# Performance work log

Measured on AMD Instinct MI355X. Metric: run time of the kernel, lower is better.

## Reference

```python
import jax, jax.numpy as jnp
import numpy as np

B, N, T = 64, 325, 12
HID = 64        # hidden_size of each expert
MEM_HID = 32    # mem_hid
MEM_SZ = 20     # memory_size
IN_DIM = 3      # input_dim
E = 3           # number of experts (len of hid_query/key/value lists)
COS_EPS = 1e-8  # torch.nn.CosineSimilarity default eps


def _xavier(key, shape):
    fan_in, fan_out = shape[-2], shape[-1]
    limit = float(np.sqrt(6.0 / (fan_in + fan_out)))
    return jax.random.uniform(key, shape, jnp.float32, -limit, limit)


def setup_inputs() -> dict:
    key = jax.random.key(0)
    ks = jax.random.split(key, 10)
    inp = {
        "input": jax.random.normal(ks[0], (B, N, T, IN_DIM), jnp.float32),
        "hidden0": jax.random.normal(ks[1], (B, N, T, HID), jnp.float32),
        "hidden1": jax.random.normal(ks[2], (B, N, T, HID), jnp.float32),
        "hidden2": jax.random.normal(ks[3], (B, N, T, HID), jnp.float32),
        # learned parameters (xavier_uniform init as in the module)
        "memory": _xavier(ks[4], (MEM_SZ, MEM_HID)),
        "input_query": _xavier(ks[5], (IN_DIM, MEM_HID)),
        # stacked per-expert projection matrices: [E, HID, MEM_HID]
        "hid_query": _xavier(ks[6], (E, HID, MEM_HID)),
        "key_w": _xavier(ks[7], (E, HID, MEM_HID)),
        "value_w": _xavier(ks[8], (E, HID, MEM_HID)),
    }
    return inp


def _cosine_sim(a, b):
    # torch CosineSimilarity(dim=-1): dot / max(||a||*||b||, eps)
    dot = jnp.sum(a * b, axis=-1)
    na = jnp.linalg.norm(a, axis=-1)
    nb = jnp.linalg.norm(b, axis=-1)
    return dot / jnp.maximum(na * nb, COS_EPS)


def reference(input, hidden0, hidden1, hidden2, memory, input_query, hid_query, key_w, value_w):
    # --- query_mem: memory-augmented representation of the raw input ---
    q = jnp.einsum('bnti,im->bntm', input, input_query)          # [B,N,T,MEM_HID]
    mem_score = jax.nn.softmax(jnp.einsum('bntm,sm->bnts', q, memory), axis=-1)
    memories = jnp.einsum('bnts,sm->bntm', mem_score, memory)    # [B,N,T,MEM_HID]

    # --- per-expert temporal self-attention in mem_hid space (vectorized over experts) ---
    h = jnp.stack([hidden0, hidden1, hidden2], axis=0)           # [E,B,N,T,HID]
    Q = jnp.einsum('ebntc,ecm->ebntm', h, hid_query)
    K = jnp.einsum('ebntc,ecm->ebntm', h, key_w)
    V = jnp.einsum('ebntc,ecm->ebntm', h, value_w)
    energy = jnp.einsum('ebntm,ebnsm->ebnts', Q, K)              # [E,B,N,T,T]
    attn = jax.nn.softmax(energy, axis=-1)
    hidden_att = jnp.einsum('ebnts,ebnsm->ebntm', attn, V)       # [E,B,N,T,MEM_HID]

    # --- cosine similarity routing scores, stacked over experts ---
    scores = _cosine_sim(memories[None], hidden_att)             # [E,B,N,T]
    return jnp.moveaxis(scores, 0, -1)                           # [B,N,T,E]
```

## Files before the change

kernel.cpp:

```cpp
#include <hip/hip_runtime.h>
#include <math.h>

typedef __attribute__((ext_vector_type(8))) short short8;
typedef __attribute__((ext_vector_type(4))) short short4v;
typedef __attribute__((ext_vector_type(4))) float f32x4;

namespace {

constexpr int kT = 12, kMS = 20, kE = 3;
constexpr int kSites = 64 * 325;
constexpr int kWaves = 8;
constexpr int kThreads = kWaves * 64;
constexpr int kNB = 340;
constexpr int kStride = kNB * kWaves;
constexpr int kIters = (kSites + kStride - 1) / kStride;

__device__ __forceinline__ void split1(float x, unsigned& hi, unsigned& lo) {
  unsigned u = __float_as_uint(x);
  hi = u >> 16;
  float r = x - __uint_as_float(u & 0xFFFF0000u);
  lo = __float_as_uint(r) >> 16;
}
__device__ __forceinline__ float btrunc(float x) {
  return __uint_as_float(__float_as_uint(x) & 0xFFFF0000u);
}
__device__ __forceinline__ unsigned pk_hi(float a, float b) {
  return __builtin_amdgcn_perm(__float_as_uint(b), __float_as_uint(a), 0x07060302u);
}
__device__ __forceinline__ unsigned pk_rnd(float a, float b) {
  return __builtin_amdgcn_perm(__float_as_uint(b) + 0x8000u,
                               __float_as_uint(a) + 0x8000u, 0x07060302u);
}

union S8 { short8 s; unsigned u[4]; };
union S4 { short4v s; unsigned u[2]; };

#define MFMA32(a, b, c) __builtin_amdgcn_mfma_f32_16x16x32_bf16((a), (b), (c), 0, 0, 0)
#define MFMA16(a, b, c) __builtin_amdgcn_mfma_f32_16x16x16bf16_1k((a), (b), (c), 0, 0, 0)

__global__ __launch_bounds__(kThreads, 4) void testam_mfma(
    const float* __restrict__ input, const float* __restrict__ h0,
    const float* __restrict__ h1, const float* __restrict__ h2,
    const float* __restrict__ memw, const float* __restrict__ iq,
    const float* __restrict__ hq, const float* __restrict__ kwt,
    const float* __restrict__ vw, float* __restrict__ out) {

  __shared__ __align__(16) unsigned short wlds[2][12][512];
  __shared__ __align__(16) float Glds[32][4];

  const int tid = threadIdx.x;
  const int e = blockIdx.x / kNB;
  const int b = blockIdx.x % kNB;
  const int l = tid & 63, wv = tid >> 6;
  const int g = l >> 4, c = l & 15;

  for (int idx = tid; idx < 768; idx += kThreads) {
    int ll = idx & 63, fi = idx >> 6;
    int mat = fi >> 2, x = (fi >> 1) & 1, y = fi & 1;
    int gg = ll >> 4, cc = ll & 15;
    const float* wp = ((mat == 0) ? hq : (mat == 1) ? kwt : vw) + e * 2048
                      + (y * 32 + gg * 8) * 32 + x * 16 + cc;
    short8 sh, sl;
    #pragma unroll
    for (int j = 0; j < 8; ++j) {
      unsigned h, lo; split1(wp[j * 32], h, lo);
      sh[j] = (short)h; sl[j] = (short)lo;
    }
    *(short8*)&wlds[0][fi][ll * 8] = sh;
    *(short8*)&wlds[1][fi][ll * 8] = sl;
  }
  for (int idx = tid; idx < 128; idx += kThreads) {
    int s = idx >> 2, d = idx & 3;
    float acc = 0.f;
    if (d < 3 && s < kMS) {
      for (int m = 0; m < 32; ++m) acc += iq[d * 32 + m] * memw[s * 32 + m];
    }
    Glds[s][d] = acc;
  }

  S4 mwh[2][2], mwl[2][2];
  #pragma unroll
  for (int p = 0; p < 2; ++p)
    #pragma unroll
    for (int sch = 0; sch < 2; ++sch) {
      float v[4];
      #pragma unroll
      for (int j = 0; j < 4; ++j) {
        int s = 16 * sch + 4 * g + j;
        v[j] = (s < kMS) ? memw[s * 32 + 16 * p + c] : 0.f;
      }
      mwh[p][sch].u[0] = pk_hi(v[0], v[1]);
      mwh[p][sch].u[1] = pk_hi(v[2], v[3]);
      mwl[p][sch].u[0] = pk_hi(v[0] - btrunc(v[0]), v[1] - btrunc(v[1]));
      mwl[p][sch].u[1] = pk_hi(v[2] - btrunc(v[2]), v[3] - btrunc(v[3]));
    }
  __syncthreads();

  const float* hbase = (e == 0) ? h0 : (e == 1) ? h1 : h2;
  const f32x4 fz = {0.f, 0.f, 0.f, 0.f};

  const int crow = (c < kT) ? c : 0;

  auto load_site = [&](int s, float* hr, float* pr) {
    const int sc_ = (s < kSites) ? s : (kSites - 1);
    const float* p = hbase + (size_t)sc_ * 768 + crow * 64 + g * 8;
    *(f32x4*)&hr[0]  = *(const f32x4*)&p[0];
    *(f32x4*)&hr[4]  = *(const f32x4*)&p[4];
    *(f32x4*)&hr[8]  = *(const f32x4*)&p[32];
    *(f32x4*)&hr[12] = *(const f32x4*)&p[36];
    const float* ip = input + (size_t)sc_ * 36 + crow * 3;
    pr[0] = ip[0]; pr[1] = ip[1]; pr[2] = ip[2];
  };

  auto body = [&](int site, const float* hv, const float* pv) {
    S8 ah[2], al[2];
    #pragma unroll
    for (int k0i = 0; k0i < 2; ++k0i)
      #pragma unroll
      for (int jj = 0; jj < 4; ++jj) {
        float a = hv[k0i * 8 + 2 * jj], bb = hv[k0i * 8 + 2 * jj + 1];
        ah[k0i].u[jj] = pk_hi(a, bb);
        al[k0i].u[jj] = pk_hi(a - btrunc(a), bb - btrunc(bb));
      }

    f32x4 cq[2] = {fz, fz}, ck[2] = {fz, fz}, cv[2] = {fz, fz};
    __builtin_amdgcn_s_setprio(1);
    #pragma unroll
    for (int p = 0; p < 2; ++p)
      #pragma unroll
      for (int k0i = 0; k0i < 2; ++k0i) {
        {
          const int fi = 0 + p * 2 + k0i;
          short8 wh = *(const short8*)&wlds[0][fi][l * 8];
          short8 wlo = *(const short8*)&wlds[1][fi][l * 8];
          cq[p] = MFMA32(wh, ah[k0i].s, cq[p]);
          cq[p] = MFMA32(wh, al[k0i].s, cq[p]);
          cq[p] = MFMA32(wlo, ah[k0i].s, cq[p]);
        }
        {
          const int fi = 4 + p * 2 + k0i;
          short8 wh = *(const short8*)&wlds[0][fi][l * 8];
          short8 wlo = *(const short8*)&wlds[1][fi][l * 8];
          ck[p] = MFMA32(wh, ah[k0i].s, ck[p]);
          ck[p] = MFMA32(wh, al[k0i].s, ck[p]);
          ck[p] = MFMA32(wlo, ah[k0i].s, ck[p]);
        }
        {
          const int fi = 8 + p * 2 + k0i;
          short8 wh = *(const short8*)&wlds[0][fi][l * 8];
          short8 wlo = *(const short8*)&wlds[1][fi][l * 8];
          cv[p] = MFMA32(ah[k0i].s, wh, cv[p]);
          cv[p] = MFMA32(ah[k0i].s, wlo, cv[p]);
          cv[p] = MFMA32(al[k0i].s, wh, cv[p]);
        }
      }
    __builtin_amdgcn_s_setprio(0);

    S4 cqh[2], cql[2], ckh[2], ckl[2], va[2];
    #pragma unroll
    for (int p = 0; p < 2; ++p) {
      cqh[p].u[0] = pk_hi(cq[p][0], cq[p][1]);
      cqh[p].u[1] = pk_hi(cq[p][2], cq[p][3]);
      cql[p].u[0] = pk_hi(cq[p][0] - btrunc(cq[p][0]), cq[p][1] - btrunc(cq[p][1]));
      cql[p].u[1] = pk_hi(cq[p][2] - btrunc(cq[p][2]), cq[p][3] - btrunc(cq[p][3]));
      ckh[p].u[0] = pk_hi(ck[p][0], ck[p][1]);
      ckh[p].u[1] = pk_hi(ck[p][2], ck[p][3]);
      ckl[p].u[0] = pk_hi(ck[p][0] - btrunc(ck[p][0]), ck[p][1] - btrunc(ck[p][1]));
      ckl[p].u[1] = pk_hi(ck[p][2] - btrunc(ck[p][2]), ck[p][3] - btrunc(ck[p][3]));
      va[p].u[0] = pk_rnd(cv[p][0], cv[p][1]);
      va[p].u[1] = pk_rnd(cv[p][2], cv[p][3]);
    }

    f32x4 eng = fz;
    #pragma unroll
    for (int p = 0; p < 2; ++p) {
      eng = MFMA16(ckh[p].s, cqh[p].s, eng);
      eng = MFMA16(ckh[p].s, cql[p].s, eng);
      eng = MFMA16(ckl[p].s, cqh[p].s, eng);
    }

    float w[4];
    {
      float mloc = -1e30f;
      if (g < 3) {
        mloc = eng[0];
        #pragma unroll
        for (int r = 1; r < 4; ++r) mloc = fmaxf(mloc, eng[r]);
      }
      float mx = mloc;
      mx = fmaxf(mx, __shfl_xor(mx, 16));
      mx = fmaxf(mx, __shfl_xor(mx, 32));
      float sloc = 0.f;
      #pragma unroll
      for (int r = 0; r < 4; ++r) {
        w[r] = (g < 3) ? __expf(eng[r] - mx) : 0.f;
        sloc += w[r];
      }
      float sm = sloc;
      sm += __shfl_xor(sm, 16);
      sm += __shfl_xor(sm, 32);
      float inv = 1.f / sm;
      #pragma unroll
      for (int r = 0; r < 4; ++r) w[r] *= inv;
    }

    S4 wh_, wl_;
    wh_.u[0] = pk_hi(w[0], w[1]);
    wh_.u[1] = pk_hi(w[2], w[3]);
    wl_.u[0] = pk_hi(w[0] - btrunc(w[0]), w[1] - btrunc(w[1]));
    wl_.u[1] = pk_hi(w[2] - btrunc(w[2]), w[3] - btrunc(w[3]));
    f32x4 hat[2];
    #pragma unroll
    for (int p = 0; p < 2; ++p) {
      hat[p] = MFMA16(va[p].s, wh_.s, fz);
      hat[p] = MFMA16(va[p].s, wl_.s, hat[p]);
    }

    float sc0[4], sc1[4];
    #pragma unroll
    for (int r = 0; r < 4; ++r) {
      const f32x4 Gv0 = *(const f32x4*)&Glds[4 * g + r][0];
      sc0[r] = pv[0] * Gv0[0] + pv[1] * Gv0[1] + pv[2] * Gv0[2];
      const f32x4 Gv1 = *(const f32x4*)&Glds[16 + 4 * g + r][0];
      sc1[r] = pv[0] * Gv1[0] + pv[1] * Gv1[1] + pv[2] * Gv1[2];
    }
    float w0[4], w1[4];
    {
      float mloc = sc0[0];
      #pragma unroll
      for (int r = 1; r < 4; ++r) mloc = fmaxf(mloc, sc0[r]);
      if (g == 0) {
        #pragma unroll
        for (int r = 0; r < 4; ++r) mloc = fmaxf(mloc, sc1[r]);
      }
      float mx = mloc;
      mx = fmaxf(mx, __shfl_xor(mx, 16));
      mx = fmaxf(mx, __shfl_xor(mx, 32));
      float sloc = 0.f;
      #pragma unroll
      for (int r = 0; r < 4; ++r) {
        w0[r] = __expf(sc0[r] - mx); sloc += w0[r];
        w1[r] = (g == 0) ? __expf(sc1[r] - mx) : 0.f; sloc += w1[r];
      }
      float sm = sloc;
      sm += __shfl_xor(sm, 16);
      sm += __shfl_xor(sm, 32);
      float inv = 1.f / sm;
      #pragma unroll
      for (int r = 0; r < 4; ++r) { w0[r] *= inv; w1[r] *= inv; }
    }

    S4 w0h, w0l, w1h, w1l;
    w0h.u[0] = pk_hi(w0[0], w0[1]);  w0h.u[1] = pk_hi(w0[2], w0[3]);
    w0l.u[0] = pk_hi(w0[0] - btrunc(w0[0]), w0[1] - btrunc(w0[1]));
    w0l.u[1] = pk_hi(w0[2] - btrunc(w0[2]), w0[3] - btrunc(w0[3]));
    w1h.u[0] = pk_hi(w1[0], w1[1]);  w1h.u[1] = pk_hi(w1[2], w1[3]);
    w1l.u[0] = pk_hi(w1[0] - btrunc(w1[0]), w1[1] - btrunc(w1[1]));
    w1l.u[1] = pk_hi(w1[2] - btrunc(w1[2]), w1[3] - btrunc(w1[3]));
    f32x4 cmem[2];
    #pragma unroll
    for (int p = 0; p < 2; ++p) {
      cmem[p] = MFMA16(mwh[p][0].s, w0h.s, fz);
      cmem[p] = MFMA16(mwh[p][0].s, w0l.s, cmem[p]);
      cmem[p] = MFMA16(mwl[p][0].s, w0h.s, cmem[p]);
      cmem[p] = MFMA16(mwh[p][1].s, w1h.s, cmem[p]);
      cmem[p] = MFMA16(mwh[p][1].s, w1l.s, cmem[p]);
      cmem[p] = MFMA16(mwl[p][1].s, w1h.s, cmem[p]);
    }

    float dot = 0.f, na = 0.f, nb = 0.f;
    #pragma unroll
    for (int p = 0; p < 2; ++p)
      #pragma unroll
      for (int r = 0; r < 4; ++r) {
        float a = cmem[p][r], h = hat[p][r];
        dot += a * h; na += a * a; nb += h * h;
      }
    dot += __shfl_xor(dot, 16); dot += __shfl_xor(dot, 32);
    na  += __shfl_xor(na, 16);  na  += __shfl_xor(na, 32);
    nb  += __shfl_xor(nb, 16);  nb  += __shfl_xor(nb, 32);
    if (g == 0 && c < kT) {
      float cvv = dot / fmaxf(sqrtf(na) * sqrtf(nb), 1e-8f);
      out[(size_t)site * (kT * kE) + c * kE + e] = cvv;
    }
  };

  float hA[16], hB[16], pA[3], pB[3];
  int site = b * kWaves + wv;
  load_site(site, hA, pA);
  for (int it = 0; it < kIters; it += 2) {
    load_site(site + kStride, hB, pB);
    if (site < kSites) body(site, hA, pA);
    load_site(site + 2 * kStride, hA, pA);
    const int s2 = site + kStride;
    if (s2 < kSites) body(s2, hB, pB);
    site += 2 * kStride;
  }
}

}

extern "C" void kernel_launch(void* const* d_in, const int* in_sizes, int n_in,
                              void* d_out, int out_size, void* d_ws, size_t ws_size,
                              hipStream_t stream) {
  const float* input = (const float*)d_in[0];
  const float* h0    = (const float*)d_in[1];
  const float* h1    = (const float*)d_in[2];
  const float* h2    = (const float*)d_in[3];
  const float* memw  = (const float*)d_in[4];
  const float* iq    = (const float*)d_in[5];
  const float* hq    = (const float*)d_in[6];
  const float* kw    = (const float*)d_in[7];
  const float* vw    = (const float*)d_in[8];
  float* out = (float*)d_out;

  testam_mfma<<<kE * kNB, kThreads, 0, stream>>>(
      input, h0, h1, h2, memw, iq, hq, kw, vw, out);
}
```

Baseline: 74.32 us.

## Process all three experts per site in one block and share the memory-branch result

```diff
diff --git a/kernel.cpp b/kernel.cpp
--- a/kernel.cpp
+++ b/kernel.cpp
@@ -11,7 +11,7 @@
 constexpr int kSites = 64 * 325;
 constexpr int kWaves = 8;
 constexpr int kThreads = kWaves * 64;
-constexpr int kNB = 340;
+constexpr int kNB = 512;
 constexpr int kStride = kNB * kWaves;
 constexpr int kIters = (kSites + kStride - 1) / kStride;
 
@@ -45,20 +45,20 @@
     const float* __restrict__ hq, const float* __restrict__ kwt,
     const float* __restrict__ vw, float* __restrict__ out) {
 
-  __shared__ __align__(16) unsigned short wlds[2][12][512];
+  __shared__ __align__(16) unsigned short wlds[kE][2][12][512];
   __shared__ __align__(16) float Glds[32][4];
 
   const int tid = threadIdx.x;
-  const int e = blockIdx.x / kNB;
-  const int b = blockIdx.x % kNB;
+  const int b = blockIdx.x;
   const int l = tid & 63, wv = tid >> 6;
   const int g = l >> 4, c = l & 15;
 
-  for (int idx = tid; idx < 768; idx += kThreads) {
-    int ll = idx & 63, fi = idx >> 6;
+  for (int idx = tid; idx < kE * 768; idx += kThreads) {
+    int e2 = idx / 768, rem = idx - e2 * 768;
+    int ll = rem & 63, fi = rem >> 6;
     int mat = fi >> 2, x = (fi >> 1) & 1, y = fi & 1;
     int gg = ll >> 4, cc = ll & 15;
-    const float* wp = ((mat == 0) ? hq : (mat == 1) ? kwt : vw) + e * 2048
+    const float* wp = ((mat == 0) ? hq : (mat == 1) ? kwt : vw) + e2 * 2048
                       + (y * 32 + gg * 8) * 32 + x * 16 + cc;
     short8 sh, sl;
     #pragma unroll
@@ -66,8 +66,8 @@
       unsigned h, lo; split1(wp[j * 32], h, lo);
       sh[j] = (short)h; sl[j] = (short)lo;
     }
-    *(short8*)&wlds[0][fi][ll * 8] = sh;
-    *(short8*)&wlds[1][fi][ll * 8] = sl;
+    *(short8*)&wlds[e2][0][fi][ll * 8] = sh;
+    *(short8*)&wlds[e2][1][fi][ll * 8] = sl;
   }
   for (int idx = tid; idx < 128; idx += kThreads) {
     int s = idx >> 2, d = idx & 3;
@@ -96,23 +96,77 @@
     }
   __syncthreads();
 
-  const float* hbase = (e == 0) ? h0 : (e == 1) ? h1 : h2;
   const f32x4 fz = {0.f, 0.f, 0.f, 0.f};
 
   const int crow = (c < kT) ? c : 0;
 
-  auto load_site = [&](int s, float* hr, float* pr) {
+  auto load_h = [&](const float* hb, int s, float* hr) {
     const int sc_ = (s < kSites) ? s : (kSites - 1);
-    const float* p = hbase + (size_t)sc_ * 768 + crow * 64 + g * 8;
+    const float* p = hb + (size_t)sc_ * 768 + crow * 64 + g * 8;
     *(f32x4*)&hr[0]  = *(const f32x4*)&p[0];
     *(f32x4*)&hr[4]  = *(const f32x4*)&p[4];
     *(f32x4*)&hr[8]  = *(const f32x4*)&p[32];
     *(f32x4*)&hr[12] = *(const f32x4*)&p[36];
+  };
+  auto load_p = [&](int s, float* pr) {
+    const int sc_ = (s < kSites) ? s : (kSites - 1);
     const float* ip = input + (size_t)sc_ * 36 + crow * 3;
     pr[0] = ip[0]; pr[1] = ip[1]; pr[2] = ip[2];
   };
 
-  auto body = [&](int site, const float* hv, const float* pv) {
+  auto memfn = [&](const float* pv, f32x4* cmem) {
+    float sc0[4], sc1[4];
+    #pragma unroll
+    for (int r = 0; r < 4; ++r) {
+      const f32x4 Gv0 = *(const f32x4*)&Glds[4 * g + r][0];
+      sc0[r] = pv[0] * Gv0[0] + pv[1] * Gv0[1] + pv[2] * Gv0[2];
+      const f32x4 Gv1 = *(const f32x4*)&Glds[16 + 4 * g + r][0];
+      sc1[r] = pv[0] * Gv1[0] + pv[1] * Gv1[1] + pv[2] * Gv1[2];
+    }
+    float w0[4], w1[4];
+    {
+      float mloc = sc0[0];
+      #pragma unroll
+      for (int r = 1; r < 4; ++r) mloc = fmaxf(mloc, sc0[r]);
+      if (g == 0) {
+        #pragma unroll
+        for (int r = 0; r < 4; ++r) mloc = fmaxf(mloc, sc1[r]);
+      }
+      float mx = mloc;
+      mx = fmaxf(mx, __shfl_xor(mx, 16));
+      mx = fmaxf(mx, __shfl_xor(mx, 32));
+      float sloc = 0.f;
+      #pragma unroll
+      for (int r = 0; r < 4; ++r) {
+        w0[r] = __expf(sc0[r] - mx); sloc += w0[r];
+        w1[r] = (g == 0) ? __expf(sc1[r] - mx) : 0.f; sloc += w1[r];
+      }
+      float sm = sloc;
+      sm += __shfl_xor(sm, 16);
+      sm += __shfl_xor(sm, 32);
+      float inv = 1.f / sm;
+      #pragma unroll
+      for (int r = 0; r < 4; ++r) { w0[r] *= inv; w1[r] *= inv; }
+    }
+    S4 w0h, w0l, w1h, w1l;
+    w0h.u[0] = pk_hi(w0[0], w0[1]);  w0h.u[1] = pk_hi(w0[2], w0[3]);
+    w0l.u[0] = pk_hi(w0[0] - btrunc(w0[0]), w0[1] - btrunc(w0[1]));
+    w0l.u[1] = pk_hi(w0[2] - btrunc(w0[2]), w0[3] - btrunc(w0[3]));
+    w1h.u[0] = pk_hi(w1[0], w1[1]);  w1h.u[1] = pk_hi(w1[2], w1[3]);
+    w1l.u[0] = pk_hi(w1[0] - btrunc(w1[0]), w1[1] - btrunc(w1[1]));
+    w1l.u[1] = pk_hi(w1[2] - btrunc(w1[2]), w1[3] - btrunc(w1[3]));
+    #pragma unroll
+    for (int p = 0; p < 2; ++p) {
+      cmem[p] = MFMA16(mwh[p][0].s, w0h.s, fz);
+      cmem[p] = MFMA16(mwh[p][0].s, w0l.s, cmem[p]);
+      cmem[p] = MFMA16(mwl[p][0].s, w0h.s, cmem[p]);
+      cmem[p] = MFMA16(mwh[p][1].s, w1h.s, cmem[p]);
+      cmem[p] = MFMA16(mwh[p][1].s, w1l.s, cmem[p]);
+      cmem[p] = MFMA16(mwl[p][1].s, w1h.s, cmem[p]);
+    }
+  };
+
+  auto body = [&](int site, int e, const float* hv, const f32x4* cmem) {
     S8 ah[2], al[2];
     #pragma unroll
     for (int k0i = 0; k0i < 2; ++k0i)
@@ -131,24 +185,24 @@
       for (int k0i = 0; k0i < 2; ++k0i) {
         {
           const int fi = 0 + p * 2 + k0i;
-          short8 wh = *(const short8*)&wlds[0][fi][l * 8];
-          short8 wlo = *(const short8*)&wlds[1][fi][l * 8];
+          short8 wh = *(const short8*)&wlds[e][0][fi][l * 8];
+          short8 wlo = *(const short8*)&wlds[e][1][fi][l * 8];
           cq[p] = MFMA32(wh, ah[k0i].s, cq[p]);
           cq[p] = MFMA32(wh, al[k0i].s, cq[p]);
           cq[p] = MFMA32(wlo, ah[k0i].s, cq[p]);
         }
         {
           const int fi = 4 + p * 2 + k0i;
-          short8 wh = *(const short8*)&wlds[0][fi][l * 8];
-          short8 wlo = *(const short8*)&wlds[1][fi][l * 8];
+          short8 wh = *(const short8*)&wlds[e][0][fi][l * 8];
+          short8 wlo = *(const short8*)&wlds[e][1][fi][l * 8];
           ck[p] = MFMA32(wh, ah[k0i].s, ck[p]);
           ck[p] = MFMA32(wh, al[k0i].s, ck[p]);
           ck[p] = MFMA32(wlo, ah[k0i].s, ck[p]);
         }
         {
           const int fi = 8 + p * 2 + k0i;
-          short8 wh = *(const short8*)&wlds[0][fi][l * 8];
-          short8 wlo = *(const short8*)&wlds[1][fi][l * 8];
+          short8 wh = *(const short8*)&wlds[e][0][fi][l * 8];
+          short8 wlo = *(const short8*)&wlds[e][1][fi][l * 8];
           cv[p] = MFMA32(ah[k0i].s, wh, cv[p]);
           cv[p] = MFMA32(ah[k0i].s, wlo, cv[p]);
           cv[p] = MFMA32(al[k0i].s, wh, cv[p]);
@@ -216,58 +270,6 @@
       hat[p] = MFMA16(va[p].s, wl_.s, hat[p]);
     }
 
-    float sc0[4], sc1[4];
-    #pragma unroll
-    for (int r = 0; r < 4; ++r) {
-      const f32x4 Gv0 = *(const f32x4*)&Glds[4 * g + r][0];
-      sc0[r] = pv[0] * Gv0[0] + pv[1] * Gv0[1] + pv[2] * Gv0[2];
-      const f32x4 Gv1 = *(const f32x4*)&Glds[16 + 4 * g + r][0];
-      sc1[r] = pv[0] * Gv1[0] + pv[1] * Gv1[1] + pv[2] * Gv1[2];
-    }
-    float w0[4], w1[4];
-    {
-      float mloc = sc0[0];
-      #pragma unroll
-      for (int r = 1; r < 4; ++r) mloc = fmaxf(mloc, sc0[r]);
-      if (g == 0) {
-        #pragma unroll
-        for (int r = 0; r < 4; ++r) mloc = fmaxf(mloc, sc1[r]);
-      }
-      float mx = mloc;
-      mx = fmaxf(mx, __shfl_xor(mx, 16));
-      mx = fmaxf(mx, __shfl_xor(mx, 32));
-      float sloc = 0.f;
-      #pragma unroll
-      for (int r = 0; r < 4; ++r) {
-        w0[r] = __expf(sc0[r] - mx); sloc += w0[r];
-        w1[r] = (g == 0) ? __expf(sc1[r] - mx) : 0.f; sloc += w1[r];
-      }
-      float sm = sloc;
-      sm += __shfl_xor(sm, 16);
-      sm += __shfl_xor(sm, 32);
-      float inv = 1.f / sm;
-      #pragma unroll
-      for (int r = 0; r < 4; ++r) { w0[r] *= inv; w1[r] *= inv; }
-    }
-
-    S4 w0h, w0l, w1h, w1l;
-    w0h.u[0] = pk_hi(w0[0], w0[1]);  w0h.u[1] = pk_hi(w0[2], w0[3]);
-    w0l.u[0] = pk_hi(w0[0] - btrunc(w0[0]), w0[1] - btrunc(w0[1]));
-    w0l.u[1] = pk_hi(w0[2] - btrunc(w0[2]), w0[3] - btrunc(w0[3]));
-    w1h.u[0] = pk_hi(w1[0], w1[1]);  w1h.u[1] = pk_hi(w1[2], w1[3]);
-    w1l.u[0] = pk_hi(w1[0] - btrunc(w1[0]), w1[1] - btrunc(w1[1]));
-    w1l.u[1] = pk_hi(w1[2] - btrunc(w1[2]), w1[3] - btrunc(w1[3]));
-    f32x4 cmem[2];
-    #pragma unroll
-    for (int p = 0; p < 2; ++p) {
-      cmem[p] = MFMA16(mwh[p][0].s, w0h.s, fz);
-      cmem[p] = MFMA16(mwh[p][0].s, w0l.s, cmem[p]);
-      cmem[p] = MFMA16(mwl[p][0].s, w0h.s, cmem[p]);
-      cmem[p] = MFMA16(mwh[p][1].s, w1h.s, cmem[p]);
-      cmem[p] = MFMA16(mwh[p][1].s, w1l.s, cmem[p]);
-      cmem[p] = MFMA16(mwl[p][1].s, w1h.s, cmem[p]);
-    }
-
     float dot = 0.f, na = 0.f, nb = 0.f;
     #pragma unroll
     for (int p = 0; p < 2; ++p)
@@ -286,14 +288,26 @@
   };
 
   float hA[16], hB[16], pA[3], pB[3];
+  f32x4 cmem[2];
   int site = b * kWaves + wv;
-  load_site(site, hA, pA);
+  load_h(h0, site, hA);
+  load_p(site, pA);
   for (int it = 0; it < kIters; it += 2) {
-    load_site(site + kStride, hB, pB);
-    if (site < kSites) body(site, hA, pA);
-    load_site(site + 2 * kStride, hA, pA);
-    const int s2 = site + kStride;
-    if (s2 < kSites) body(s2, hB, pB);
+    const int s1 = site, s2 = site + kStride;
+    load_h(h1, s1, hB);
+    if (s1 < kSites) { memfn(pA, cmem); body(s1, 0, hA, cmem); }
+    load_h(h2, s1, hA);
+    if (s1 < kSites) body(s1, 1, hB, cmem);
+    load_h(h0, s2, hB);
+    load_p(s2, pB);
+    if (s1 < kSites) body(s1, 2, hA, cmem);
+    load_h(h1, s2, hA);
+    if (s2 < kSites) { memfn(pB, cmem); body(s2, 0, hB, cmem); }
+    load_h(h2, s2, hB);
+    if (s2 < kSites) body(s2, 1, hA, cmem);
+    load_h(h0, s2 + kStride, hA);
+    load_p(s2 + kStride, pA);
+    if (s2 < kSites) body(s2, 2, hB, cmem);
     site += 2 * kStride;
   }
 }
@@ -314,6 +328,6 @@
   const float* vw    = (const float*)d_in[8];
   float* out = (float*)d_out;
 
-  testam_mfma<<<kE * kNB, kThreads, 0, stream>>>(
+  testam_mfma<<<kNB, kThreads, 0, stream>>>(
       input, h0, h1, h2, memw, iq, hq, kw, vw, out);
 }
```

Result: faster. 65.68 us, median of 2 (-11.6%).
